# Kernel tuning notes

Measured on AMD Instinct MI355X. Metric: run time of the kernel, lower is better.

Reference implementation:

```python
import jax, jax.numpy as jnp
import numpy as np

N, D, M_COLS, K = 4096, 512, 4096, 2048

def setup_inputs() -> dict:
    key = jax.random.key(0)
    k1, k2, k3 = jax.random.split(key, 3)
    return {
        "in_activations": jax.random.normal(k1, (N, D), dtype=jnp.float32),
        "M": jax.random.normal(k2, (D, M_COLS), dtype=jnp.float32),
        "centroids": jax.random.normal(k3, (K, D), dtype=jnp.float32),
    }

def reference(in_activations, M, centroids):
    # dist[k, m] = || X @ (M[:, m] - c_k) ||_2  over the n sampled activations.
    # Expand || a - b ||^2 = ||a||^2 - 2 a.b + ||b||^2 with a = X@M[:,m], b = X@c_k
    # to avoid materializing the [K, n, m] broadcast tensor of the original.
    XM = in_activations @ M                 # [n, m]
    XC = in_activations @ centroids.T      # [n, K]
    sq = (jnp.sum(XM * XM, axis=0)[None, :]          # [1, m]
          - 2.0 * (XC.T @ XM)                        # [K, m]
          + jnp.sum(XC * XC, axis=0)[:, None])       # [K, 1]
    return jnp.sqrt(jnp.maximum(sq, 0.0))            # [K, m]
```

## Files before the change

kernel.cpp:

```cpp
#include <hip/hip_runtime.h>
#include <stdint.h>

#define NR    4096
#define D_DIM 512
#define MC    4096
#define KC    2048

typedef unsigned short u16;
typedef __attribute__((ext_vector_type(8))) short bf16x8;
typedef __attribute__((ext_vector_type(4))) float f32x4;

__device__ __forceinline__ u16 f2bf(float f) {
  union { float f; uint32_t u; } v; v.f = f;
  return (u16)((v.u + 0x7FFFu + ((v.u >> 16) & 1u)) >> 16);
}
__device__ __forceinline__ float bf2f(u16 h) {
  union { uint32_t u; float f; } v; v.u = (uint32_t)h << 16; return v.f;
}
__device__ __forceinline__ void gload16(const void* g, void* lds) {
  __builtin_amdgcn_global_load_lds((const __attribute__((address_space(1))) void*)g,
                                   (__attribute__((address_space(3))) void*)lds,
                                   16, 0, 0);
}

template <int EPI>
__device__ __forceinline__ void gemm_tile(
    const u16* __restrict__ Ag, const u16* __restrict__ Bg,
    float* __restrict__ Cf, u16* __restrict__ Cbf,
    const u16* __restrict__ DotH, const float* __restrict__ DotF,
    float* __restrict__ vatom, const float* __restrict__ tv, const float* __restrict__ sv,
    int m0, int n0, int Ndim, int Kdim, int kBeg, int kEnd,
    u16* As, u16* Bs, int tid)
{
  const int rowt = tid >> 3;
  const int colt = (tid & 7) << 3;
  const int wave = tid >> 6, lane = tid & 63;
  const int wr = (wave >> 1) << 6, wc = (wave & 1) << 6;
  const int fr = lane & 15, fk = (lane >> 4) << 3;
  char* AsB = (char*)As;
  char* BsB = (char*)Bs;
  const int wb = wave << 10;

  f32x4 acc[4][4] = {};

  for (int k0 = kBeg; k0 < kEnd; k0 += 64) {
    const u16* ag = Ag + (size_t)(m0 + rowt) * Kdim + k0 + colt;
    const u16* bg = Bg + (size_t)(n0 + rowt) * Kdim + k0 + colt;
    #pragma unroll
    for (int c = 0; c < 4; ++c) {
      gload16(ag + (size_t)(c * 32) * Kdim, AsB + c * 4096 + wb);
      gload16(bg + (size_t)(c * 32) * Kdim, BsB + c * 4096 + wb);
    }
    __syncthreads();
    #pragma unroll
    for (int kk = 0; kk < 64; kk += 32) {
      bf16x8 a[4], b[4];
      #pragma unroll
      for (int i = 0; i < 4; ++i) a[i] = *(const bf16x8*)&As[(size_t)(wr + i * 16 + fr) * 64 + kk + fk];
      #pragma unroll
      for (int j = 0; j < 4; ++j) b[j] = *(const bf16x8*)&Bs[(size_t)(wc + j * 16 + fr) * 64 + kk + fk];
      #pragma unroll
      for (int i = 0; i < 4; ++i)
        #pragma unroll
        for (int j = 0; j < 4; ++j)
          acc[i][j] = __builtin_amdgcn_mfma_f32_16x16x32_bf16(a[i], b[j], acc[i][j], 0, 0, 0);
    }
    __syncthreads();
  }

  const int q = lane >> 4;
  #pragma unroll
  for (int i = 0; i < 4; ++i) {
    #pragma unroll
    for (int r = 0; r < 4; ++r) {
      const int grow = m0 + wr + i * 16 + q * 4 + r;
      float p = 0.f;
      #pragma unroll
      for (int j = 0; j < 4; ++j) {
        const int gcol = n0 + wc + j * 16 + fr;
        const float v = acc[i][j][r];
        const size_t idx = (size_t)grow * Ndim + gcol;
        if (EPI == 0) Cf[idx] = v;
        if (EPI == 2) { float sq = tv[gcol] - 2.f * v + sv[grow]; Cf[idx] = sqrtf(fmaxf(sq, 0.f)); }
        if (EPI == 3) { Cbf[idx] = f2bf(v); p += v * bf2f(DotH[idx]); }
        if (EPI == 4) { p += v * DotF[idx]; }
      }
      if (EPI == 3 || EPI == 4) {
        #pragma unroll
        for (int off = 1; off < 16; off <<= 1) p += __shfl_xor(p, off);
        if (fr == 0) atomicAdd(&vatom[grow], p);
      }
    }
  }
}

__device__ __forceinline__ void transpose_tile(
    const float* __restrict__ in, u16* __restrict__ out, int R, int C,
    int rt, int ct, int tid, float* tile )
{
  const int tx = tid & 31, ty = tid >> 5;
  #pragma unroll
  for (int i = 0; i < 32; i += 8)
    tile[(size_t)(ty + i) * 33 + tx] = in[(size_t)(rt + ty + i) * C + ct + tx];
  __syncthreads();
  #pragma unroll
  for (int i = 0; i < 32; i += 8)
    out[(size_t)(ct + ty + i) * R + rt + tx] = f2bf(tile[(size_t)tx * 33 + ty + i]);
  __syncthreads();
}

__global__ __launch_bounds__(256)
void prep(const float* __restrict__ X, const float* __restrict__ Mm,
          const float* __restrict__ Cc,
          u16* __restrict__ XT_bf, u16* __restrict__ M_bfT, u16* __restrict__ C_bf,
          float* __restrict__ tvec)
{
  __shared__ float tile[32 * 33];
  const int b = blockIdx.x, tid = threadIdx.x;
  if (b < 512) {
    #pragma unroll 1
    for (int j = 0; j < 4; ++j) {
      int T = b * 4 + j;
      transpose_tile(X, XT_bf, NR, D_DIM, (T >> 4) * 32, (T & 15) * 32, tid, tile);
    }
  } else if (b < 1024) {
    #pragma unroll 1
    for (int j = 0; j < 4; ++j) {
      int T = (b - 512) * 4 + j;
      transpose_tile(Mm, M_bfT, D_DIM, MC, (T >> 7) * 32, (T & 127) * 32, tid, tile);
    }
  } else {
    const int bb = b - 1024;
    int zi = bb * 256 + tid;
    if (zi < 4096 + 2048) tvec[zi] = 0.f;
    const float4* C4 = (const float4*)Cc;
    #pragma unroll 1
    for (int i = bb * 256 + tid; i < (KC * D_DIM) / 4; i += 128 * 256) {
      float4 v = C4[i];
      ushort4 r; r.x = f2bf(v.x); r.y = f2bf(v.y); r.z = f2bf(v.z); r.w = f2bf(v.w);
      *(ushort4*)&C_bf[(size_t)i * 4] = r;
    }
  }
}

__global__ __launch_bounds__(256)
void g_gemm(const u16* __restrict__ XT_bf, float* __restrict__ Gpart)
{
  __shared__ __align__(16) u16 As[128 * 64];
  __shared__ __align__(16) u16 Bs[128 * 64];
  const int t = blockIdx.x, z = blockIdx.y;
  const int n0 = (t & 3) * 128, m0 = (t >> 2) * 128;
  gemm_tile<0>(XT_bf, XT_bf, Gpart + (size_t)z * 512 * 512, nullptr, nullptr, nullptr,
               nullptr, nullptr, nullptr, m0, n0, 512, NR, z * 512, z * 512 + 512,
               As, Bs, threadIdx.x);
}

__global__ __launch_bounds__(256)
void reduce_g(const float* __restrict__ Gpart, u16* __restrict__ G_bf)
{
  const float4* P4 = (const float4*)Gpart;
  int i = blockIdx.x * 256 + threadIdx.x;
  float4 s = {0.f, 0.f, 0.f, 0.f};
  #pragma unroll
  for (int z = 0; z < 8; ++z) {
    float4 v = P4[(size_t)z * (512 * 512 / 4) + i];
    s.x += v.x; s.y += v.y; s.z += v.z; s.w += v.w;
  }
  ushort4 r; r.x = f2bf(s.x); r.y = f2bf(s.y); r.z = f2bf(s.z); r.w = f2bf(s.w);
  *(ushort4*)&G_bf[(size_t)i * 4] = r;
}

__global__ __launch_bounds__(256)
void mid(const u16* __restrict__ M_bfT, const u16* __restrict__ C_bf,
         const u16* __restrict__ G_bf, const float* __restrict__ Cc,
         u16* __restrict__ A_bfT, float* __restrict__ tvec)
{
  __shared__ __align__(16) u16 As[128 * 64];
  __shared__ __align__(16) u16 Bs[128 * 64];
  const int b = blockIdx.x, tid = threadIdx.x;
  if (b < 128) {
    const int n0 = (b & 3) * 128, m0 = (b >> 2) * 128;
    gemm_tile<3>(M_bfT, G_bf, nullptr, A_bfT, M_bfT, nullptr, tvec, nullptr, nullptr,
                 m0, n0, 512, 512, 0, 512, As, Bs, tid);
  } else {
    const int u = b - 128;
    const int n0 = (u & 3) * 128, m0 = (u >> 2) * 128;
    gemm_tile<4>(C_bf, G_bf, nullptr, nullptr, nullptr, Cc, tvec + 4096, nullptr, nullptr,
                 m0, n0, 512, 512, 0, 512, As, Bs, tid);
  }
}

__global__ __launch_bounds__(256)
void final_gemm(const u16* __restrict__ C_bf, const u16* __restrict__ A_bfT,
                const float* __restrict__ tvec, float* __restrict__ out)
{
  __shared__ __align__(16) u16 As[128 * 64];
  __shared__ __align__(16) u16 Bs[128 * 64];
  const int n0 = blockIdx.x * 128, m0 = blockIdx.y * 128;
  gemm_tile<2>(C_bf, A_bfT, out, nullptr, nullptr, nullptr, nullptr, tvec, tvec + 4096,
               m0, n0, MC, 512, 0, 512, As, Bs, threadIdx.x);
}

extern "C" void kernel_launch(void* const* d_in, const int* in_sizes, int n_in,
                              void* d_out, int out_size, void* d_ws, size_t ws_size,
                              hipStream_t stream) {
  const float* X  = (const float*)d_in[0];
  const float* Mm = (const float*)d_in[1];
  const float* Cc = (const float*)d_in[2];
  float* out = (float*)d_out;

  char* ws = (char*)d_ws;
  const size_t MB = 1u << 20;
  u16*   XT_bf = (u16*)(ws);
  u16*   C_bf  = (u16*)(ws + 4 * MB);
  u16*   M_bfT = (u16*)(ws + 6 * MB);
  u16*   A_bfT = (u16*)(ws + 10 * MB);
  u16*   G_bf  = (u16*)(ws + 14 * MB);
  float* tvec  = (float*)(ws + 14 * MB + 512 * 1024);
  float* Gpart = (float*)(ws + 15 * MB);

  prep<<<1152, 256, 0, stream>>>(X, Mm, Cc, XT_bf, M_bfT, C_bf, tvec);
  g_gemm<<<dim3(16, 8), 256, 0, stream>>>(XT_bf, Gpart);
  reduce_g<<<256, 256, 0, stream>>>(Gpart, G_bf);
  mid<<<192, 256, 0, stream>>>(M_bfT, C_bf, G_bf, Cc, A_bfT, tvec);
  final_gemm<<<dim3(32, 16), 256, 0, stream>>>(C_bf, A_bfT, tvec, out);
}
```

Before: 133.5 us.

## Fuse split-K Gram GEMM and reduction via in-kernel grid barrier

```diff
diff --git a/kernel.cpp b/kernel.cpp
--- a/kernel.cpp
+++ b/kernel.cpp
@@ -144,30 +144,47 @@
 }
 
 __global__ __launch_bounds__(256)
-void g_gemm(const u16* __restrict__ XT_bf, float* __restrict__ Gpart)
+void gk(const u16* __restrict__ XT_bf, float* __restrict__ Gpart,
+        u16* __restrict__ G_bf, unsigned* __restrict__ cnt)
 {
   __shared__ __align__(16) u16 As[128 * 64];
   __shared__ __align__(16) u16 Bs[128 * 64];
-  const int t = blockIdx.x, z = blockIdx.y;
+  const int tid = threadIdx.x;
+  const int t = blockIdx.x & 15, z = blockIdx.x >> 4;
   const int n0 = (t & 3) * 128, m0 = (t >> 2) * 128;
   gemm_tile<0>(XT_bf, XT_bf, Gpart + (size_t)z * 512 * 512, nullptr, nullptr, nullptr,
                nullptr, nullptr, nullptr, m0, n0, 512, NR, z * 512, z * 512 + 512,
-               As, Bs, threadIdx.x);
-}
-
-__global__ __launch_bounds__(256)
-void reduce_g(const float* __restrict__ Gpart, u16* __restrict__ G_bf)
-{
-  const float4* P4 = (const float4*)Gpart;
-  int i = blockIdx.x * 256 + threadIdx.x;
-  float4 s = {0.f, 0.f, 0.f, 0.f};
-  #pragma unroll
-  for (int z = 0; z < 8; ++z) {
-    float4 v = P4[(size_t)z * (512 * 512 / 4) + i];
-    s.x += v.x; s.y += v.y; s.z += v.z; s.w += v.w;
-  }
-  ushort4 r; r.x = f2bf(s.x); r.y = f2bf(s.y); r.z = f2bf(s.z); r.w = f2bf(s.w);
-  *(ushort4*)&G_bf[(size_t)i * 4] = r;
+               As, Bs, tid);
+
+  __syncthreads();
+  if (tid == 0) {
+    __threadfence();
+    atomicAdd(cnt, 1u);
+    long spin = 0;
+    while (__hip_atomic_load(cnt, __ATOMIC_ACQUIRE, __HIP_MEMORY_SCOPE_AGENT) < 128u) {
+      __builtin_amdgcn_s_sleep(2);
+      if (++spin > (1L << 27)) break;
+    }
+    __threadfence();
+  }
+  __syncthreads();
+
+  {
+    const int i0 = (blockIdx.x * 256 + tid) * 8;
+    float s[8] = {0.f, 0.f, 0.f, 0.f, 0.f, 0.f, 0.f, 0.f};
+    #pragma unroll
+    for (int zz = 0; zz < 8; ++zz) {
+      const float4* p = (const float4*)&Gpart[(size_t)zz * 512 * 512 + i0];
+      float4 a = p[0], b = p[1];
+      s[0] += a.x; s[1] += a.y; s[2] += a.z; s[3] += a.w;
+      s[4] += b.x; s[5] += b.y; s[6] += b.z; s[7] += b.w;
+    }
+    ushort4 r0, r1;
+    r0.x = f2bf(s[0]); r0.y = f2bf(s[1]); r0.z = f2bf(s[2]); r0.w = f2bf(s[3]);
+    r1.x = f2bf(s[4]); r1.y = f2bf(s[5]); r1.z = f2bf(s[6]); r1.w = f2bf(s[7]);
+    *(ushort4*)&G_bf[i0] = r0;
+    *(ushort4*)&G_bf[i0 + 4] = r1;
+  }
 }
 
 __global__ __launch_bounds__(256)
@@ -218,10 +235,11 @@
   u16*   G_bf  = (u16*)(ws + 14 * MB);
   float* tvec  = (float*)(ws + 14 * MB + 512 * 1024);
   float* Gpart = (float*)(ws + 15 * MB);
-
+  unsigned* barcnt = (unsigned*)(ws + 31 * MB);
+
+  hipMemsetAsync(barcnt, 0, sizeof(unsigned), stream);
   prep<<<1152, 256, 0, stream>>>(X, Mm, Cc, XT_bf, M_bfT, C_bf, tvec);
-  g_gemm<<<dim3(16, 8), 256, 0, stream>>>(XT_bf, Gpart);
-  reduce_g<<<256, 256, 0, stream>>>(Gpart, G_bf);
+  gk<<<128, 256, 0, stream>>>(XT_bf, Gpart, G_bf, barcnt);
   mid<<<192, 256, 0, stream>>>(M_bfT, C_bf, G_bf, Cc, A_bfT, tvec);
   final_gemm<<<dim3(32, 16), 256, 0, stream>>>(C_bf, A_bfT, tvec, out);
 }
```

After: 148.2 us. 1.11x slower.

## Double-buffer LDS tiles with XOR swizzle and deepen split-K for Gram GEMM

Applied to the files above, without the earlier changes.

```diff
diff --git a/kernel.cpp b/kernel.cpp
--- a/kernel.cpp
+++ b/kernel.cpp
@@ -30,35 +30,48 @@
     const u16* __restrict__ DotH, const float* __restrict__ DotF,
     float* __restrict__ vatom, const float* __restrict__ tv, const float* __restrict__ sv,
     int m0, int n0, int Ndim, int Kdim, int kBeg, int kEnd,
-    u16* As, u16* Bs, int tid)
+    u16* As0, u16* As1, u16* Bs0, u16* Bs1, int tid)
 {
   const int rowt = tid >> 3;
-  const int colt = (tid & 7) << 3;
+  const int cswz = ((tid & 7) ^ ((tid >> 3) & 7)) << 3;
   const int wave = tid >> 6, lane = tid & 63;
   const int wr = (wave >> 1) << 6, wc = (wave & 1) << 6;
-  const int fr = lane & 15, fk = (lane >> 4) << 3;
-  char* AsB = (char*)As;
-  char* BsB = (char*)Bs;
+  const int fr = lane & 15;
+  const int sw = fr & 7;
+  const int hq = lane >> 4;
   const int wb = wave << 10;
 
   f32x4 acc[4][4] = {};
-
-  for (int k0 = kBeg; k0 < kEnd; k0 += 64) {
-    const u16* ag = Ag + (size_t)(m0 + rowt) * Kdim + k0 + colt;
-    const u16* bg = Bg + (size_t)(n0 + rowt) * Kdim + k0 + colt;
-    #pragma unroll
-    for (int c = 0; c < 4; ++c) {
-      gload16(ag + (size_t)(c * 32) * Kdim, AsB + c * 4096 + wb);
-      gload16(bg + (size_t)(c * 32) * Kdim, BsB + c * 4096 + wb);
-    }
-    __syncthreads();
+  const u16* agB = Ag + (size_t)(m0 + rowt) * Kdim + cswz;
+  const u16* bgB = Bg + (size_t)(n0 + rowt) * Kdim + cswz;
+
+  #define STAGE(k0, Asb, Bsb)                                          \
+    _Pragma("unroll")                                                  \
+    for (int c = 0; c < 4; ++c) {                                      \
+      gload16(agB + (k0) + (size_t)(c * 32) * Kdim, (char*)(Asb) + c * 4096 + wb); \
+      gload16(bgB + (k0) + (size_t)(c * 32) * Kdim, (char*)(Bsb) + c * 4096 + wb); \
+    }
+
+  STAGE(kBeg, As0, Bs0)
+  __syncthreads();
+
+  const int nt = (kEnd - kBeg) >> 6;
+  for (int t = 0; t < nt; ++t) {
+    u16* Ac = (t & 1) ? As1 : As0;
+    u16* Bc = (t & 1) ? Bs1 : Bs0;
+    if (t + 1 < nt) {
+      u16* An = (t & 1) ? As0 : As1;
+      u16* Bn = (t & 1) ? Bs0 : Bs1;
+      STAGE(kBeg + (t + 1) * 64, An, Bn)
+    }
     #pragma unroll
     for (int kk = 0; kk < 64; kk += 32) {
+      const int so = ((((kk >> 3) + hq) ^ sw) << 3);
       bf16x8 a[4], b[4];
       #pragma unroll
-      for (int i = 0; i < 4; ++i) a[i] = *(const bf16x8*)&As[(size_t)(wr + i * 16 + fr) * 64 + kk + fk];
-      #pragma unroll
-      for (int j = 0; j < 4; ++j) b[j] = *(const bf16x8*)&Bs[(size_t)(wc + j * 16 + fr) * 64 + kk + fk];
+      for (int i = 0; i < 4; ++i) a[i] = *(const bf16x8*)&Ac[(wr + i * 16 + fr) * 64 + so];
+      #pragma unroll
+      for (int j = 0; j < 4; ++j) b[j] = *(const bf16x8*)&Bc[(wc + j * 16 + fr) * 64 + so];
       #pragma unroll
       for (int i = 0; i < 4; ++i)
         #pragma unroll
@@ -67,6 +80,7 @@
     }
     __syncthreads();
   }
+  #undef STAGE
 
   const int q = lane >> 4;
   #pragma unroll
@@ -146,13 +160,13 @@
 __global__ __launch_bounds__(256)
 void g_gemm(const u16* __restrict__ XT_bf, float* __restrict__ Gpart)
 {
-  __shared__ __align__(16) u16 As[128 * 64];
-  __shared__ __align__(16) u16 Bs[128 * 64];
+  __shared__ __align__(16) u16 As[2][8192];
+  __shared__ __align__(16) u16 Bs[2][8192];
   const int t = blockIdx.x, z = blockIdx.y;
   const int n0 = (t & 3) * 128, m0 = (t >> 2) * 128;
   gemm_tile<0>(XT_bf, XT_bf, Gpart + (size_t)z * 512 * 512, nullptr, nullptr, nullptr,
-               nullptr, nullptr, nullptr, m0, n0, 512, NR, z * 512, z * 512 + 512,
-               As, Bs, threadIdx.x);
+               nullptr, nullptr, nullptr, m0, n0, 512, NR, z * 256, z * 256 + 256,
+               As[0], As[1], Bs[0], Bs[1], threadIdx.x);
 }
 
 __global__ __launch_bounds__(256)
@@ -162,7 +176,7 @@
   int i = blockIdx.x * 256 + threadIdx.x;
   float4 s = {0.f, 0.f, 0.f, 0.f};
   #pragma unroll
-  for (int z = 0; z < 8; ++z) {
+  for (int z = 0; z < 16; ++z) {
     float4 v = P4[(size_t)z * (512 * 512 / 4) + i];
     s.x += v.x; s.y += v.y; s.z += v.z; s.w += v.w;
   }
@@ -175,18 +189,18 @@
          const u16* __restrict__ G_bf, const float* __restrict__ Cc,
          u16* __restrict__ A_bfT, float* __restrict__ tvec)
 {
-  __shared__ __align__(16) u16 As[128 * 64];
-  __shared__ __align__(16) u16 Bs[128 * 64];
+  __shared__ __align__(16) u16 As[2][8192];
+  __shared__ __align__(16) u16 Bs[2][8192];
   const int b = blockIdx.x, tid = threadIdx.x;
   if (b < 128) {
     const int n0 = (b & 3) * 128, m0 = (b >> 2) * 128;
     gemm_tile<3>(M_bfT, G_bf, nullptr, A_bfT, M_bfT, nullptr, tvec, nullptr, nullptr,
-                 m0, n0, 512, 512, 0, 512, As, Bs, tid);
+                 m0, n0, 512, 512, 0, 512, As[0], As[1], Bs[0], Bs[1], tid);
   } else {
     const int u = b - 128;
     const int n0 = (u & 3) * 128, m0 = (u >> 2) * 128;
     gemm_tile<4>(C_bf, G_bf, nullptr, nullptr, nullptr, Cc, tvec + 4096, nullptr, nullptr,
-                 m0, n0, 512, 512, 0, 512, As, Bs, tid);
+                 m0, n0, 512, 512, 0, 512, As[0], As[1], Bs[0], Bs[1], tid);
   }
 }
 
@@ -194,11 +208,11 @@
 void final_gemm(const u16* __restrict__ C_bf, const u16* __restrict__ A_bfT,
                 const float* __restrict__ tvec, float* __restrict__ out)
 {
-  __shared__ __align__(16) u16 As[128 * 64];
-  __shared__ __align__(16) u16 Bs[128 * 64];
+  __shared__ __align__(16) u16 As[2][8192];
+  __shared__ __align__(16) u16 Bs[2][8192];
   const int n0 = blockIdx.x * 128, m0 = blockIdx.y * 128;
   gemm_tile<2>(C_bf, A_bfT, out, nullptr, nullptr, nullptr, nullptr, tvec, tvec + 4096,
-               m0, n0, MC, 512, 0, 512, As, Bs, threadIdx.x);
+               m0, n0, MC, 512, 0, 512, As[0], As[1], Bs[0], Bs[1], threadIdx.x);
 }
 
 extern "C" void kernel_launch(void* const* d_in, const int* in_sizes, int n_in,
@@ -220,7 +234,7 @@
   float* Gpart = (float*)(ws + 15 * MB);
 
   prep<<<1152, 256, 0, stream>>>(X, Mm, Cc, XT_bf, M_bfT, C_bf, tvec);
-  g_gemm<<<dim3(16, 8), 256, 0, stream>>>(XT_bf, Gpart);
+  g_gemm<<<dim3(16, 16), 256, 0, stream>>>(XT_bf, Gpart);
   reduce_g<<<256, 256, 0, stream>>>(Gpart, G_bf);
   mid<<<192, 256, 0, stream>>>(M_bfT, C_bf, G_bf, Cc, A_bfT, tvec);
   final_gemm<<<dim3(32, 16), 256, 0, stream>>>(C_bf, A_bfT, tvec, out);
```

After: 130.6 us. 2.2% less time.
